# Kernel optimization log

Hardware: AMD Instinct MI355X
Metric: run time of the kernel (lower is better)

Reference implementation:

```python
import jax, jax.numpy as jnp
import numpy as np
import math


def setup_inputs() -> dict:
    key = jax.random.key(0)
    ks = jax.random.split(key, 10)
    b, n, d, h = 2, 1024, 1024, 16
    hd = d // h
    std = 0.02
    x = jax.random.normal(ks[0], (b, n, d), jnp.float32)
    Wq = jax.random.normal(ks[1], (d, d), jnp.float32) * std
    Wk = jax.random.normal(ks[2], (d, d), jnp.float32) * std
    Wv = jax.random.normal(ks[3], (d, d), jnp.float32) * std
    Wo = jax.random.normal(ks[4], (d, d), jnp.float32) * std
    Ww1 = jax.random.normal(ks[5], (d, hd), jnp.float32) * std
    Ww2 = jax.random.normal(ks[6], (hd, d), jnp.float32) * std
    Wb = jax.random.normal(ks[7], (d, h), jnp.float32) * std
    Wf = jax.random.normal(ks[8], (d, h), jnp.float32) * std
    # delta initialized so sigmoid(delta) = threshold = 0.99
    delta = jnp.full((h,), math.log(0.99 / (1.0 - 0.99)), jnp.float32)
    return dict(x=x, Wq=Wq, Wk=Wk, Wv=Wv, Wo=Wo, Ww1=Ww1, Ww2=Ww2, Wb=Wb, Wf=Wf, delta=delta)


def reference(x, Wq, Wk, Wv, Wo, Ww1, Ww2, Wb, Wf, delta):
    b, n, d = x.shape
    h = delta.shape[0]
    hd = d // h
    scale = hd ** -0.5
    q = (x @ Wq).reshape(b, n, h, hd)
    k = (x @ Wk).reshape(b, n, h, hd)
    v = (x @ Wv).reshape(b, n, h, hd)
    w = ((x @ Ww1) @ Ww2).reshape(b, n, h, hd)
    # l2-normalize write directions per head
    w = w * jax.lax.rsqrt(jnp.sum(w * w, axis=-1, keepdims=True) + 1e-6)
    beta = 2.0 * jax.nn.sigmoid(x @ Wb)                      # (b,n,h)
    log_f = jax.nn.log_sigmoid((x @ Wf + delta).astype(jnp.float32))  # (b,n,h)
    bt = jnp.transpose(beta, (0, 2, 1))                      # (b,h,n)
    # PaTH attention: logit_{t,j} = q_t^T H_t H_{t-1} ... H_{j+1} k_j, H_s = I - beta_s w_s w_s^T.
    # UT transform: c_{s,j} = w_s . k_j^{(s-1)} satisfies (I + L) C = tril(W K^T, -1)
    # with L_{s,r} = beta_r (w_s . w_r) for r < s.
    A = jnp.einsum('bshd,brhd->bhsr', w, w)                  # w_s . w_r
    L = jnp.tril(A, -1) * bt[:, :, None, :]                  # (b,h,n,n), strictly lower
    Mlow = jnp.tril(jnp.einsum('bshd,bjhd->bhsj', w, k), -1)
    C = jax.scipy.linalg.solve_triangular(L, Mlow, lower=True, unit_diagonal=True)
    # transformed score: S_{t,j} = q_t.k_j - sum_{j<s<=t} beta_s (q_t.w_s) c_{s,j}
    G = jnp.tril(jnp.einsum('bthd,bshd->bhts', q, w) * bt[:, :, None, :])
    S = jnp.einsum('bthd,bjhd->bhtj', q, k) - G @ C          # (b,h,n,n)
    # forgetting-gate decay: add F_t - F_j (cumulative log-sigmoid gates)
    Fc = jnp.cumsum(jnp.transpose(log_f, (0, 2, 1)), axis=-1)  # (b,h,n)
    logits = S * scale + Fc[..., :, None] - Fc[..., None, :]
    mask = jnp.tril(jnp.ones((n, n), bool))
    logits = jnp.where(mask, logits, -jnp.inf)
    P = jax.nn.softmax(logits, axis=-1)
    o = jnp.einsum('bhtj,bjhd->bthd', P, v).reshape(b, n, d)
    return o @ Wo
```

## Files before the change

kernel.cpp:

```cpp
#include <hip/hip_runtime.h>
#include <hip/hip_bf16.h>

#define DEV static __device__ __forceinline__

constexpr float SM_SCALE = 0.125f;

typedef __attribute__((ext_vector_type(8))) short s16x8;
typedef __attribute__((ext_vector_type(8))) unsigned short u16x8;
typedef __attribute__((ext_vector_type(4))) unsigned short u16x4;
typedef __attribute__((ext_vector_type(4))) float f32x4;

DEV float bf2f(unsigned short u) {
  union { unsigned int i; float f; } v; v.i = ((unsigned int)u) << 16; return v.f;
}
DEV unsigned short f2bf(float f) {
  union { float f; unsigned int i; } v; v.f = f;
  unsigned int r = v.i + 0x7fffu + ((v.i >> 16) & 1u);
  return (unsigned short)(r >> 16);
}
DEV void tri_unrank(int r, int& k, int& i) {
  k = (int)((sqrtf(8.f * r + 1.f) - 1.f) * 0.5f);
  while (k * (k + 1) / 2 > r) --k;
  while ((k + 1) * (k + 2) / 2 <= r) ++k;
  i = r - k * (k + 1) / 2;
}
DEV void glds16(const void* g, void* l) {
  __builtin_amdgcn_global_load_lds(
      (const __attribute__((address_space(1))) void*)g,
      (__attribute__((address_space(3))) void*)l, 16, 0, 0);
}
DEV void pipe_drain_barrier() {
  asm volatile("s_waitcnt vmcnt(0)" ::: "memory");
  __builtin_amdgcn_s_barrier();
}

constexpr size_t OFF_XB   = 0;
constexpr size_t OFF_WQT  = 4194304;
constexpr size_t OFF_WKT  = 6291456;
constexpr size_t OFF_WVT  = 8388608;
constexpr size_t OFF_WOT  = 10485760;
constexpr size_t OFF_W1C  = 12582912;
constexpr size_t OFF_W2T  = 12713984;
constexpr size_t OFF_BETA = 12582912;
constexpr size_t OFF_Q16  = 12845056;
constexpr size_t OFF_K16  = 17039360;
constexpr size_t OFF_VT   = 21233664;
constexpr size_t OFF_WN16 = 25427968;
constexpr size_t OFF_WB16 = 29622272;
constexpr size_t OFF_WNF  = 33816576;
constexpr size_t OFF_OB   = 33816576;
constexpr size_t OFF_BFT  = 38010880;
constexpr size_t OFF_FC   = 38273024;
constexpr size_t OFF_L    = 38404096;
constexpr size_t OFF_CT   = 105512960;
constexpr size_t OFF_G    = 172621824;
constexpr size_t OFF_BL   = 239730688;
constexpr size_t OFF_U128 = 244187136;
constexpr size_t OFF_B256 = 252575744;

__global__ __launch_bounds__(256) void prep_all(
    const float* __restrict__ W0, const float* __restrict__ W1,
    const float* __restrict__ W2, const float* __restrict__ W3,
    const float* __restrict__ Ww1, const float* __restrict__ Ww2,
    const float* __restrict__ x, const float* __restrict__ Wb,
    const float* __restrict__ Wf,
    unsigned short* __restrict__ D0, unsigned short* __restrict__ D1,
    unsigned short* __restrict__ D2, unsigned short* __restrict__ D3,
    unsigned short* __restrict__ W1c, unsigned short* __restrict__ W2T,
    unsigned short* __restrict__ xb, unsigned short* __restrict__ BFT) {
  int bidx = blockIdx.x;
  int t = threadIdx.x;
  if (bidx >= 2096) {
    int e0 = ((bidx - 2096) * 256 + t) * 8;
    int j = e0 >> 10, i0 = e0 & 1023;
    u16x8 o;
#pragma unroll
    for (int e = 0; e < 8; ++e) {
      int i = i0 + e;
      float v = 0.f;
      if (j < 16) v = Wb[i * 16 + j];
      else if (j < 32) v = Wf[i * 16 + (j - 16)];
      o[e] = f2bf(v);
    }
    *(u16x8*)(BFT + e0) = o;
    return;
  }
  if (bidx >= 2064) {
    int i = ((bidx - 2064) * 256 + t) * 8;
    float4 a = *(const float4*)(Ww1 + i);
    float4 b = *(const float4*)(Ww1 + i + 4);
    u16x8 o;
    o[0] = f2bf(a.x); o[1] = f2bf(a.y); o[2] = f2bf(a.z); o[3] = f2bf(a.w);
    o[4] = f2bf(b.x); o[5] = f2bf(b.y); o[6] = f2bf(b.z); o[7] = f2bf(b.w);
    *(u16x8*)(W1c + i) = o;
    return;
  }
  if (bidx >= 1040) {
    int i = ((bidx - 1040) * 256 + t) * 8;
    float4 a = *(const float4*)(x + i);
    float4 b = *(const float4*)(x + i + 4);
    u16x8 o;
    o[0] = f2bf(a.x); o[1] = f2bf(a.y); o[2] = f2bf(a.z); o[3] = f2bf(a.w);
    o[4] = f2bf(b.x); o[5] = f2bf(b.y); o[6] = f2bf(b.z); o[7] = f2bf(b.w);
    *(u16x8*)(xb + i) = o;
    return;
  }
  const float* src; unsigned short* dst; int R, C, c0, r0;
  if (bidx >= 1024) {
    src = Ww2; dst = W2T; R = 64; C = 1024;
    c0 = (bidx - 1024) * 64; r0 = 0;
  } else {
    int z = bidx >> 8, xy = bidx & 255;
    src = z == 0 ? W0 : z == 1 ? W1 : z == 2 ? W2 : W3;
    dst = z == 0 ? D0 : z == 1 ? D1 : z == 2 ? D2 : D3;
    R = 1024; C = 1024;
    c0 = (xy & 15) * 64; r0 = (xy >> 4) * 64;
  }
  __shared__ float tile[64 * 65];
#pragma unroll
  for (int i = 0; i < 16; ++i) {
    int lin = t + i * 256; int r = lin >> 6, c = lin & 63;
    tile[r * 65 + c] = src[(size_t)(r0 + r) * C + c0 + c];
  }
  __syncthreads();
#pragma unroll
  for (int i = 0; i < 16; ++i) {
    int lin = t + i * 256; int c = lin >> 6, r = lin & 63;
    dst[(size_t)(c0 + c) * R + r0 + r] = f2bf(tile[r * 65 + c]);
  }
}

__global__ __launch_bounds__(256) void bgfc(const float* __restrict__ BL,
    const float* __restrict__ delta, float* __restrict__ Beta, float* __restrict__ Fc) {
  int bh = blockIdx.x;
  int b = bh >> 4, h = bh & 15;
  int t = threadIdx.x;
  __shared__ float buf[1024];
  __shared__ float tsum[256];
  float dh = delta[h];
#pragma unroll
  for (int i = 0; i < 4; ++i) {
    int n = t + i * 256;
    int row = (b << 10) + n;
    float braw = BL[row * 64 + h];
    Beta[row * 16 + h] = 2.f / (1.f + __expf(-braw));
    float lraw = BL[row * 64 + 16 + h] + dh;
    buf[n] = (lraw >= 0.f) ? -log1pf(__expf(-lraw)) : (lraw - log1pf(__expf(lraw)));
  }
  __syncthreads();
  float loc[4]; float run = 0.f;
#pragma unroll
  for (int i = 0; i < 4; ++i) { run += buf[t * 4 + i]; loc[i] = run; }
  tsum[t] = run;
  __syncthreads();
  for (int off = 1; off < 256; off <<= 1) {
    float add = (t >= off) ? tsum[t - off] : 0.f;
    __syncthreads();
    tsum[t] += add;
    __syncthreads();
  }
  float excl = tsum[t] - run;
#pragma unroll
  for (int i = 0; i < 4; ++i) Fc[bh * 1024 + t * 4 + i] = excl + loc[i];
}

__global__ __launch_bounds__(256) void proj_big(const unsigned short* __restrict__ xb,
    const unsigned short* __restrict__ WqT, const unsigned short* __restrict__ WkT,
    const unsigned short* __restrict__ WvT, const unsigned short* __restrict__ WfT,
    const unsigned short* __restrict__ BFT,
    unsigned short* __restrict__ Q16, unsigned short* __restrict__ K16,
    unsigned short* __restrict__ VT, unsigned short* __restrict__ WNF,
    float* __restrict__ BL) {
  int sg = blockIdx.x;
  int virt = (sg % 8) * 66 + (sg / 8);
  const unsigned short *A, *BT; unsigned short* out = nullptr; int m0, n0;
  int mode = 0;
  if (virt < 256) {
    int g = virt >> 4, in = virt & 15;
    int ssb = g >> 2, gin = g & 3;
    int mb = (ssb >> 1) * 2 + (gin >> 1);
    int nb = (ssb & 1) * 2 + (gin & 1);
    int my = mb * 4 + (in >> 2);
    int nx = nb * 4 + (in & 3);
    m0 = my * 128; A = xb;
    if (nx < 8) { BT = WqT; out = Q16; n0 = nx * 128; }
    else { BT = WkT; out = K16; n0 = (nx - 8) * 128; }
  } else if (virt < 384) {
    int r = virt - 256; int bz = r >> 6; int rr = r & 63;
    int g = rr >> 4, in = rr & 15;
    int my = (g >> 1) * 4 + (in >> 2);
    int nx = (g & 1) * 4 + (in & 3);
    m0 = my * 128; n0 = nx * 128;
    A = WvT; BT = xb + ((size_t)bz << 20); out = VT + ((size_t)bz << 20);
  } else if (virt < 512) {
    int r = virt - 384;
    int g = r >> 4, in = r & 15;
    int my = (g >> 1) * 4 + (in >> 2);
    int nx = (g & 1) * 4 + (in & 3);
    m0 = my * 128; n0 = nx * 128;
    A = xb; BT = WfT; out = WNF;
  } else {
    m0 = (virt - 512) * 128; n0 = 0;
    A = xb; BT = BFT; mode = 1;
  }
  int t = threadIdx.x;
  int w = t >> 6, l = t & 63;
  int wr = w >> 1, wc = w & 1;
  int fr = l & 15, fq = l >> 4;
  __shared__ unsigned short As[2 * 8192];
  __shared__ unsigned short Bs[2 * 8192];
  f32x4 acc[4][4];
#pragma unroll
  for (int m = 0; m < 4; ++m)
#pragma unroll
    for (int c = 0; c < 4; ++c) acc[m][c] = (f32x4){0.f, 0.f, 0.f, 0.f};

#define STAGE_PB(buf, k0) {                                             \
  _Pragma("unroll")                                                     \
  for (int i = 0; i < 4; ++i) {                                         \
    int cid = t + i * 256;                                              \
    int row = cid >> 3, ch = cid & 7;                                   \
    int chs = ch ^ (row & 7);                                           \
    glds16(A + (size_t)(m0 + row) * 1024 + (k0) + chs * 8, (char*)(As + (buf) * 8192) + cid * 16); \
    glds16(BT + (size_t)(n0 + row) * 1024 + (k0) + chs * 8, (char*)(Bs + (buf) * 8192) + cid * 16); \
  } }

  STAGE_PB(0, 0);
  pipe_drain_barrier();
  int cur = 0;
  for (int kt = 0; kt < 16; ++kt) {
    if (kt < 15) STAGE_PB(cur ^ 1, (kt + 1) * 64);
    const char* Ab = (const char*)(As + cur * 8192);
    const char* Bb = (const char*)(Bs + cur * 8192);
    __builtin_amdgcn_s_setprio(1);
#pragma unroll
    for (int kh = 0; kh < 2; ++kh) {
      s16x8 af[4], bfv[4];
#pragma unroll
      for (int m = 0; m < 4; ++m) {
        int ra = wr * 64 + 16 * m + fr;
        af[m] = *(const s16x8*)(Ab + (((ra << 7) + (kh << 6) + (fq << 4)) ^ ((ra & 7) << 4)));
      }
#pragma unroll
      for (int c = 0; c < 4; ++c) {
        int rb = wc * 64 + 16 * c + fr;
        bfv[c] = *(const s16x8*)(Bb + (((rb << 7) + (kh << 6) + (fq << 4)) ^ ((rb & 7) << 4)));
      }
#pragma unroll
      for (int m = 0; m < 4; ++m)
#pragma unroll
        for (int c = 0; c < 4; ++c)
          acc[m][c] = __builtin_amdgcn_mfma_f32_16x16x32_bf16(af[m], bfv[c], acc[m][c], 0, 0, 0);
    }
    __builtin_amdgcn_s_setprio(0);
    pipe_drain_barrier();
    cur ^= 1;
  }
#undef STAGE_PB
#pragma unroll
  for (int m = 0; m < 4; ++m) {
#pragma unroll
    for (int c = 0; c < 4; ++c) {
      int col = n0 + wc * 64 + 16 * c + fr;
#pragma unroll
      for (int r = 0; r < 4; ++r) {
        int grow = m0 + wr * 64 + 16 * m + fq * 4 + r;
        if (mode == 0) out[(size_t)grow * 1024 + col] = f2bf(acc[m][c][r]);
        else if (col < 64) BL[(size_t)grow * 64 + col] = acc[m][c][r];
      }
    }
  }
}

template<int F32OUT>
__global__ __launch_bounds__(256) void gemm_nt(const unsigned short* __restrict__ A,
    const unsigned short* __restrict__ BT, void* __restrict__ out,
    int M, int N, int K) {
  __shared__ unsigned short As[2 * 4096];
  __shared__ unsigned short Bs[2 * 4096];
  int m0 = blockIdx.y * 64, n0 = blockIdx.x * 64;
  int t = threadIdx.x;
  int w = t >> 6, l = t & 63, fr = l & 15;
  int koB = (l >> 4) * 16;
  f32x4 acc[4];
#pragma unroll
  for (int c = 0; c < 4; ++c) acc[c] = (f32x4){0.f, 0.f, 0.f, 0.f};

#define STAGE_G(buf, k0) {                                              \
  _Pragma("unroll")                                                     \
  for (int i = 0; i < 2; ++i) {                                         \
    int cid = t + i * 256;                                              \
    int row = cid >> 3, ch = cid & 7;                                   \
    int chs = ch ^ (row & 7);                                           \
    glds16(A + (size_t)(m0 + row) * K + (k0) + chs * 8, (char*)(As + (buf) * 4096) + cid * 16); \
    glds16(BT + (size_t)(n0 + row) * K + (k0) + chs * 8, (char*)(Bs + (buf) * 4096) + cid * 16); \
  } }

  int nt = K >> 6;
  STAGE_G(0, 0);
  pipe_drain_barrier();
  int cur = 0;
  for (int kt = 0; kt < nt; ++kt) {
    if (kt + 1 < nt) STAGE_G(cur ^ 1, (kt + 1) * 64);
    const char* Ab = (const char*)(As + cur * 4096);
    const char* Bb = (const char*)(Bs + cur * 4096);
    __builtin_amdgcn_s_setprio(1);
#pragma unroll
    for (int kh = 0; kh < 2; ++kh) {
      int ra = 16 * w + fr;
      s16x8 a = *(const s16x8*)(Ab + (((ra << 7) + (kh << 6) + koB) ^ ((ra & 7) << 4)));
#pragma unroll
      for (int c = 0; c < 4; ++c) {
        int rb = 16 * c + fr;
        s16x8 bb = *(const s16x8*)(Bb + (((rb << 7) + (kh << 6) + koB) ^ ((rb & 7) << 4)));
        acc[c] = __builtin_amdgcn_mfma_f32_16x16x32_bf16(a, bb, acc[c], 0, 0, 0);
      }
    }
    __builtin_amdgcn_s_setprio(0);
    pipe_drain_barrier();
    cur ^= 1;
  }
#undef STAGE_G
  int rbase = m0 + 16 * w + ((l >> 4) << 2);
#pragma unroll
  for (int c = 0; c < 4; ++c) {
    int col = n0 + 16 * c + fr;
#pragma unroll
    for (int r = 0; r < 4; ++r) {
      if (F32OUT) ((float*)out)[(size_t)(rbase + r) * N + col] = acc[c][r];
      else ((unsigned short*)out)[(size_t)(rbase + r) * N + col] = f2bf(acc[c][r]);
    }
  }
}

__global__ __launch_bounds__(256) void gemm_outproj(const unsigned short* __restrict__ A,
    const unsigned short* __restrict__ BT, float* __restrict__ out) {
  int sg = blockIdx.x;
  int virt = (sg & 7) * 64 + (sg >> 3);
  int g = virt >> 6, in = virt & 63;
  int my = (g >> 1) * 8 + (in >> 3);
  int nx = (g & 1) * 8 + (in & 7);
  int m0 = my * 64, n0 = nx * 64;
  const int K = 1024, N = 1024;
  __shared__ unsigned short As[2 * 4096];
  __shared__ unsigned short Bs[2 * 4096];
  int t = threadIdx.x;
  int w = t >> 6, l = t & 63, fr = l & 15;
  int koB = (l >> 4) * 16;
  f32x4 acc[4];
#pragma unroll
  for (int c = 0; c < 4; ++c) acc[c] = (f32x4){0.f, 0.f, 0.f, 0.f};

#define STAGE_O(buf, k0) {                                              \
  _Pragma("unroll")                                                     \
  for (int i = 0; i < 2; ++i) {                                         \
    int cid = t + i * 256;                                              \
    int row = cid >> 3, ch = cid & 7;                                   \
    int chs = ch ^ (row & 7);                                           \
    glds16(A + (size_t)(m0 + row) * K + (k0) + chs * 8, (char*)(As + (buf) * 4096) + cid * 16); \
    glds16(BT + (size_t)(n0 + row) * K + (k0) + chs * 8, (char*)(Bs + (buf) * 4096) + cid * 16); \
  } }

  STAGE_O(0, 0);
  pipe_drain_barrier();
  int cur = 0;
  for (int kt = 0; kt < 16; ++kt) {
    if (kt + 1 < 16) STAGE_O(cur ^ 1, (kt + 1) * 64);
    const char* Ab = (const char*)(As + cur * 4096);
    const char* Bb = (const char*)(Bs + cur * 4096);
    __builtin_amdgcn_s_setprio(1);
#pragma unroll
    for (int kh = 0; kh < 2; ++kh) {
      int ra = 16 * w + fr;
      s16x8 a = *(const s16x8*)(Ab + (((ra << 7) + (kh << 6) + koB) ^ ((ra & 7) << 4)));
#pragma unroll
      for (int c = 0; c < 4; ++c) {
        int rb = 16 * c + fr;
        s16x8 bb = *(const s16x8*)(Bb + (((rb << 7) + (kh << 6) + koB) ^ ((rb & 7) << 4)));
        acc[c] = __builtin_amdgcn_mfma_f32_16x16x32_bf16(a, bb, acc[c], 0, 0, 0);
      }
    }
    __builtin_amdgcn_s_setprio(0);
    pipe_drain_barrier();
    cur ^= 1;
  }
#undef STAGE_O
  int rbase = m0 + 16 * w + ((l >> 4) << 2);
#pragma unroll
  for (int c = 0; c < 4; ++c) {
    int col = n0 + 16 * c + fr;
#pragma unroll
    for (int r = 0; r < 4; ++r)
      out[(size_t)(rbase + r) * N + col] = acc[c][r];
  }
}

__global__ __launch_bounds__(256) void wnorm2(const unsigned short* __restrict__ WNF,
    const float* __restrict__ Beta, unsigned short* __restrict__ WN,
    unsigned short* __restrict__ WB) {
  int row = blockIdx.x;
  int wave = threadIdx.x >> 6, lane = threadIdx.x & 63;
#pragma unroll
  for (int i = 0; i < 4; ++i) {
    int hh = wave * 4 + i;
    size_t idx = ((size_t)row << 10) + hh * 64 + lane;
    float v = bf2f(WNF[idx]);
    float ss = v * v;
#pragma unroll
    for (int off = 1; off < 64; off <<= 1) ss += __shfl_xor(ss, off);
    float wn = v * rsqrtf(ss + 1e-6f);
    WN[idx] = f2bf(wn);
    WB[idx] = f2bf(wn * Beta[row * 16 + hh]);
  }
}

__global__ __launch_bounds__(256) void pairLG(const unsigned short* __restrict__ WN,
    const unsigned short* __restrict__ Q, const unsigned short* __restrict__ WB,
    unsigned short* __restrict__ Lg, unsigned short* __restrict__ Gg) {
  int idx = blockIdx.x;
  int bh = idx & 31, r0r = idx >> 5;
  int tb2, jb2; tri_unrank(r0r, tb2, jb2);
  int b = bh >> 4, h = bh & 15;
  int m0 = tb2 * 128, n0 = jb2 * 128;
  int t = threadIdx.x;
  int w = t >> 6, l = t & 63;
  int wr = w >> 1, wc = w & 1;
  int fr = l & 15, fq = l >> 4;
  __shared__ unsigned short As[128 * 64];
  __shared__ unsigned short Bs[128 * 64];
  const unsigned short* WNb = WN + ((size_t)b << 20) + h * 64;
  const unsigned short* Qb  = Q + ((size_t)b << 20) + h * 64;
  const unsigned short* WBb = WB + ((size_t)b << 20) + h * 64;
  size_t base = (size_t)bh << 20;
#pragma unroll
  for (int i = 0; i < 4; ++i) {
    int cid = t + i * 256;
    int row = cid >> 3, ch = cid & 7;
    int chs = ch ^ (row & 7);
    glds16(WNb + ((size_t)(m0 + row) << 10) + chs * 8, (char*)As + cid * 16);
    glds16(WBb + ((size_t)(n0 + row) << 10) + chs * 8, (char*)Bs + cid * 16);
  }
  __syncthreads();
  for (int pass = 0; pass < 2; ++pass) {
    f32x4 acc[4][4];
#pragma unroll
    for (int m = 0; m < 4; ++m)
#pragma unroll
      for (int c = 0; c < 4; ++c) acc[m][c] = (f32x4){0.f, 0.f, 0.f, 0.f};
#pragma unroll
    for (int kh = 0; kh < 2; ++kh) {
      s16x8 af[4], bfv[4];
#pragma unroll
      for (int m = 0; m < 4; ++m) {
        int ra = wr * 64 + 16 * m + fr;
        af[m] = *(const s16x8*)((char*)As + (((ra << 7) + (kh << 6) + (fq << 4)) ^ ((ra & 7) << 4)));
      }
#pragma unroll
      for (int c = 0; c < 4; ++c) {
        int rb = wc * 64 + 16 * c + fr;
        bfv[c] = *(const s16x8*)((char*)Bs + (((rb << 7) + (kh << 6) + (fq << 4)) ^ ((rb & 7) << 4)));
      }
#pragma unroll
      for (int m = 0; m < 4; ++m)
#pragma unroll
        for (int c = 0; c < 4; ++c)
          acc[m][c] = __builtin_amdgcn_mfma_f32_16x16x32_bf16(af[m], bfv[c], acc[m][c], 0, 0, 0);
    }
    unsigned short* dst = pass ? Gg : Lg;
#pragma unroll
    for (int m = 0; m < 4; ++m) {
#pragma unroll
      for (int c = 0; c < 4; ++c) {
        int gj = n0 + wc * 64 + 16 * c + fr;
#pragma unroll
        for (int r = 0; r < 4; ++r) {
          int gi = m0 + wr * 64 + 16 * m + fq * 4 + r;
          bool keep = pass ? (gj <= gi) : (gj < gi);
          dst[base + ((size_t)gi << 10) + gj] = f2bf(keep ? -acc[m][c][r] : 0.f);
        }
      }
    }
    if (pass == 0) {
      __syncthreads();
#pragma unroll
      for (int i = 0; i < 4; ++i) {
        int cid = t + i * 256;
        int row = cid >> 3, ch = cid & 7;
        int chs = ch ^ (row & 7);
        glds16(Qb + ((size_t)(m0 + row) << 10) + chs * 8, (char*)As + cid * 16);
      }
      __syncthreads();
    }
  }
}

__global__ __launch_bounds__(256) void score128s(const unsigned short* __restrict__ Q,
    const unsigned short* __restrict__ Kk, const unsigned short* __restrict__ G,
    const unsigned short* __restrict__ CT, unsigned short* __restrict__ Sg) {
  int idx = blockIdx.x;
  int bh = idx & 31, r0r = idx >> 5;
  int k, i; tri_unrank(r0r, k, i);
  int tb2 = (7 - k) + i, jb2 = i;
  int b = bh >> 4, h = bh & 15;
  int m0 = tb2 * 128, n0 = jb2 * 128;
  int t = threadIdx.x;
  int w = t >> 6, l = t & 63;
  int wr = w >> 1, wc = w & 1;
  int fr = l & 15, fq = l >> 4;
  __shared__ unsigned short As[2 * 8192];
  __shared__ unsigned short Bs[2 * 8192];
  size_t base = (size_t)bh << 20;
  const unsigned short* Qb_ = Q + ((size_t)b << 20) + h * 64;
  const unsigned short* Kb_ = Kk + ((size_t)b << 20) + h * 64;
  const unsigned short* Gb_ = G + base;
  const unsigned short* Cb_ = CT + base;
  int kbase = jb2 * 128;
  int nsteps = 1 + (tb2 - jb2 + 1) * 2;
  f32x4 acc[4][4];
#pragma unroll
  for (int m = 0; m < 4; ++m)
#pragma unroll
    for (int c = 0; c < 4; ++c) acc[m][c] = (f32x4){0.f, 0.f, 0.f, 0.f};

#define STAGE_SC(buf, stp) {                                            \
  const unsigned short* pa; const unsigned short* pb; int koff;         \
  if ((stp) == 0) { pa = Qb_; pb = Kb_; koff = 0; }                     \
  else { pa = Gb_; pb = Cb_; koff = kbase + ((stp) - 1) * 64; }         \
  _Pragma("unroll")                                                     \
  for (int i2 = 0; i2 < 4; ++i2) {                                      \
    int cid = t + i2 * 256;                                             \
    int row = cid >> 3, ch = cid & 7;                                   \
    int chs = ch ^ (row & 7);                                           \
    glds16(pa + ((size_t)(m0 + row) << 10) + koff + chs * 8, (char*)(As + (buf) * 8192) + cid * 16); \
    glds16(pb + ((size_t)(n0 + row) << 10) + koff + chs * 8, (char*)(Bs + (buf) * 8192) + cid * 16); \
  } }

  STAGE_SC(0, 0);
  pipe_drain_barrier();
  int cur = 0;
  for (int step = 0; step < nsteps; ++step) {
    if (step + 1 < nsteps) STAGE_SC(cur ^ 1, step + 1);
    const char* Ab = (const char*)(As + cur * 8192);
    const char* Bb = (const char*)(Bs + cur * 8192);
    __builtin_amdgcn_s_setprio(1);
#pragma unroll
    for (int kh = 0; kh < 2; ++kh) {
      s16x8 af[4], bfv[4];
#pragma unroll
      for (int m = 0; m < 4; ++m) {
        int ra = wr * 64 + 16 * m + fr;
        af[m] = *(const s16x8*)(Ab + (((ra << 7) + (kh << 6) + (fq << 4)) ^ ((ra & 7) << 4)));
      }
#pragma unroll
      for (int c = 0; c < 4; ++c) {
        int rb = wc * 64 + 16 * c + fr;
        bfv[c] = *(const s16x8*)(Bb + (((rb << 7) + (kh << 6) + (fq << 4)) ^ ((rb & 7) << 4)));
      }
#pragma unroll
      for (int m = 0; m < 4; ++m)
#pragma unroll
        for (int c = 0; c < 4; ++c)
          acc[m][c] = __builtin_amdgcn_mfma_f32_16x16x32_bf16(af[m], bfv[c], acc[m][c], 0, 0, 0);
    }
    __builtin_amdgcn_s_setprio(0);
    pipe_drain_barrier();
    cur ^= 1;
  }
#undef STAGE_SC
#pragma unroll
  for (int m = 0; m < 4; ++m) {
#pragma unroll
    for (int c = 0; c < 4; ++c) {
      int gj = n0 + wc * 64 + 16 * c + fr;
#pragma unroll
      for (int r = 0; r < 4; ++r) {
        int gi = m0 + wr * 64 + 16 * m + fq * 4 + r;
        Sg[base + ((size_t)gi << 10) + gj] = f2bf(acc[m][c][r]);
      }
    }
  }
}

__global__ __launch_bounds__(256) void invbuild(const unsigned short* __restrict__ Lb,
    unsigned short* __restrict__ U128) {
  int ib = blockIdx.x, bh = blockIdx.y;
  int t = threadIdx.x, w = t >> 6, l = t & 63, fr = l & 15, fq = l >> 4;
  int s0 = ib * 128;
  size_t base = (size_t)bh << 20;
  unsigned short* Uo = U128 + (((size_t)(bh * 8 + ib)) << 14);
  __shared__ float LD[2][64 * 65];
  __shared__ unsigned short UaR[64 * 72];
  __shared__ unsigned short UcR[64 * 72];
  __shared__ unsigned short UaT[64 * 64];
  __shared__ unsigned short T1T[64 * 64];
#pragma unroll
  for (int i = 0; i < 32; ++i) {
    int lin = t + i * 256;
    int blk = lin >> 12, s = (lin >> 6) & 63, r = lin & 63;
    LD[blk][s * 65 + r] = -bf2f(Lb[base + ((size_t)(s0 + blk * 64 + s) << 10) + s0 + blk * 64 + r]);
  }
  __syncthreads();
  if (t < 128) {
    int blk = t >> 6, j = t & 63;
    const float* ld = LD[blk];
    float cc[64];
#pragma unroll
    for (int s = 0; s < 64; ++s) cc[s] = (s == j) ? 1.f : 0.f;
#pragma unroll
    for (int r = 0; r < 63; ++r) {
      float val = cc[r];
#pragma unroll
      for (int s = r + 1; s < 64; ++s) cc[s] -= ld[s * 65 + r] * val;
    }
    if (blk == 0) {
#pragma unroll
      for (int s = 0; s < 64; ++s) {
        unsigned short v = f2bf(cc[s]);
        UaR[s * 72 + j] = v;
        *(unsigned short*)((char*)UaT + (((j << 7) + (s << 1)) ^ ((j & 7) << 4))) = v;
      }
    } else {
#pragma unroll
      for (int s = 0; s < 64; ++s) UcR[s * 72 + j] = f2bf(cc[s]);
    }
  }
  __syncthreads();
#pragma unroll
  for (int i = 0; i < 8; ++i) {
    int cid = t + i * 256;
    int row = cid >> 4, ch = cid & 15;
    u16x8 v = {0, 0, 0, 0, 0, 0, 0, 0};
    if (row < 64) {
      if (ch < 8) {
#pragma unroll
        for (int e = 0; e < 8; ++e) v[e] = UaR[row * 72 + ch * 8 + e];
      }
      *(u16x8*)(Uo + row * 128 + ch * 8) = v;
    } else if (ch >= 8) {
#pragma unroll
      for (int e = 0; e < 8; ++e) v[e] = UcR[(row - 64) * 72 + (ch - 8) * 8 + e];
      *(u16x8*)(Uo + row * 128 + ch * 8) = v;
    }
  }
  f32x4 a1[4];
#pragma unroll
  for (int c = 0; c < 4; ++c) a1[c] = (f32x4){0.f, 0.f, 0.f, 0.f};
#pragma unroll
  for (int kc = 0; kc < 2; ++kc) {
    s16x8 af = *(const s16x8*)(Lb + base + ((size_t)(s0 + 64 + 16 * w + fr) << 10) + s0 + kc * 32 + fq * 8);
#pragma unroll
    for (int c = 0; c < 4; ++c) {
      int j = 16 * c + fr;
      s16x8 bb = *(const s16x8*)((char*)UaT + (((j << 7) + (kc << 6) + (fq << 4)) ^ ((j & 7) << 4)));
      a1[c] = __builtin_amdgcn_mfma_f32_16x16x32_bf16(af, bb, a1[c], 0, 0, 0);
    }
  }
#pragma unroll
  for (int c = 0; c < 4; ++c) {
    int gj = 16 * c + fr;
    int sb = 16 * w + fq * 4;
    u16x4 pk;
#pragma unroll
    for (int r = 0; r < 4; ++r) pk[r] = f2bf(a1[c][r]);
    *(u16x4*)((char*)T1T + (((gj << 7) + (sb << 1)) ^ ((gj & 7) << 4))) = pk;
  }
  __syncthreads();
  f32x4 a2[4];
#pragma unroll
  for (int c = 0; c < 4; ++c) a2[c] = (f32x4){0.f, 0.f, 0.f, 0.f};
#pragma unroll
  for (int kc = 0; kc < 2; ++kc) {
    s16x8 af = *(const s16x8*)(UcR + (16 * w + fr) * 72 + kc * 32 + fq * 8);
#pragma unroll
    for (int c = 0; c < 4; ++c) {
      int j = 16 * c + fr;
      s16x8 bb = *(const s16x8*)((char*)T1T + (((j << 7) + (kc << 6) + (fq << 4)) ^ ((j & 7) << 4)));
      a2[c] = __builtin_amdgcn_mfma_f32_16x16x32_bf16(af, bb, a2[c], 0, 0, 0);
    }
  }
#pragma unroll
  for (int c = 0; c < 4; ++c) {
    int gj = 16 * c + fr;
#pragma unroll
    for (int r = 0; r < 4; ++r)
      Uo[(64 + 16 * w + fq * 4 + r) * 128 + gj] = f2bf(a2[c][r]);
  }
}

__global__ __launch_bounds__(256) void u256build(const unsigned short* __restrict__ Lb,
    const unsigned short* __restrict__ U128, unsigned short* __restrict__ B256) {
  int qb = blockIdx.x, bh = blockIdx.y;
  int t = threadIdx.x, w = t >> 6, l = t & 63, fr = l & 15, fq = l >> 4;
  int s0 = qb * 256;
  size_t base = (size_t)bh << 20;
  const unsigned short* Ua = U128 + (((size_t)(bh * 8 + 2 * qb)) << 14);
  const unsigned short* Uc = U128 + (((size_t)(bh * 8 + 2 * qb + 1)) << 14);
  unsigned short* out = B256 + (((size_t)(bh * 4 + qb)) << 14);
  __shared__ unsigned short UaT[16384];
  __shared__ unsigned short T1T[16384];
#pragma unroll
  for (int i = 0; i < 8; ++i) {
    int cid = t + i * 256;
    int s = cid >> 4, ch = cid & 15;
    u16x8 v = *(const u16x8*)(Ua + s * 128 + ch * 8);
#pragma unroll
    for (int e = 0; e < 8; ++e) {
      int j = ch * 8 + e;
      int byt = ((j << 8) + (s << 1)) ^ ((j & 15) << 4);
      *(unsigned short*)((char*)UaT + byt) = v[e];
    }
  }
  __syncthreads();
  f32x4 a1[2][8];
#pragma unroll
  for (int m = 0; m < 2; ++m)
#pragma unroll
    for (int c = 0; c < 8; ++c) a1[m][c] = (f32x4){0.f, 0.f, 0.f, 0.f};
#pragma unroll
  for (int kc = 0; kc < 4; ++kc) {
    s16x8 af[2];
#pragma unroll
    for (int m = 0; m < 2; ++m)
      af[m] = *(const s16x8*)(Lb + base + ((size_t)(s0 + 128 + 32 * w + 16 * m + fr) << 10) + s0 + kc * 32 + fq * 8);
#pragma unroll
    for (int c = 0; c < 8; ++c) {
      int j = 16 * c + fr;
      s16x8 bb = *(const s16x8*)((char*)UaT + (((j << 8) + (kc << 6) + (fq << 4)) ^ ((j & 15) << 4)));
#pragma unroll
      for (int m = 0; m < 2; ++m)
        a1[m][c] = __builtin_amdgcn_mfma_f32_16x16x32_bf16(af[m], bb, a1[m][c], 0, 0, 0);
    }
  }
#pragma unroll
  for (int m = 0; m < 2; ++m) {
#pragma unroll
    for (int c = 0; c < 8; ++c) {
      int col = 16 * c + fr;
      int row0 = 32 * w + 16 * m + fq * 4;
      u16x4 pk;
#pragma unroll
      for (int r = 0; r < 4; ++r) pk[r] = f2bf(a1[m][c][r]);
      int byt = ((col << 8) + (row0 << 1)) ^ ((col & 15) << 4);
      *(u16x4*)((char*)T1T + byt) = pk;
    }
  }
  __syncthreads();
  f32x4 a2[2][8];
#pragma unroll
  for (int m = 0; m < 2; ++m)
#pragma unroll
    for (int c = 0; c < 8; ++c) a2[m][c] = (f32x4){0.f, 0.f, 0.f, 0.f};
#pragma unroll
  for (int kc = 0; kc < 4; ++kc) {
    s16x8 af[2];
#pragma unroll
    for (int m = 0; m < 2; ++m)
      af[m] = *(const s16x8*)(Uc + (32 * w + 16 * m + fr) * 128 + kc * 32 + fq * 8);
#pragma unroll
    for (int c = 0; c < 8; ++c) {
      int j = 16 * c + fr;
      s16x8 bb = *(const s16x8*)((char*)T1T + (((j << 8) + (kc << 6) + (fq << 4)) ^ ((j & 15) << 4)));
#pragma unroll
      for (int m = 0; m < 2; ++m)
        a2[m][c] = __builtin_amdgcn_mfma_f32_16x16x32_bf16(af[m], bb, a2[m][c], 0, 0, 0);
    }
  }
#pragma unroll
  for (int m = 0; m < 2; ++m) {
#pragma unroll
    for (int c = 0; c < 8; ++c) {
      int col = 16 * c + fr;
#pragma unroll
      for (int r = 0; r < 4; ++r)
        out[(32 * w + 16 * m + fq * 4 + r) * 128 + col] = f2bf(a2[m][c][r]);
    }
  }
}

__global__ __launch_bounds__(256) void solve256(const unsigned short* __restrict__ WN,
    const unsigned short* __restrict__ Kk, const unsigned short* __restrict__ Lb,
    const unsigned short* __restrict__ U128, const unsigned short* __restrict__ B256,
    unsigned short* __restrict__ CT, int ib) {
  int jb = blockIdx.x, bh = blockIdx.y;
  int b = bh >> 4, h = bh & 15;
  int t = threadIdx.x, w = t >> 6, l = t & 63, fr = l & 15, fq = l >> 4;
  int s0 = ib * 256, j0 = jb * 128;
  size_t base = (size_t)bh << 20;
  __shared__ unsigned short sh[49152];
  unsigned short* rT = sh;
  const unsigned short* Wb_ = WN + ((size_t)b << 20) + h * 64;
  const unsigned short* Kb_ = Kk + ((size_t)b << 20) + h * 64;

  f32x4 acc[4][8];
#pragma unroll
  for (int m = 0; m < 4; ++m)
#pragma unroll
    for (int c = 0; c < 8; ++c) acc[m][c] = (f32x4){0.f, 0.f, 0.f, 0.f};
  int nst = 1 + 4 * ib - 2 * jb; if (nst < 1) nst = 1;

#define STAGE_SV(buf, stp) {                                            \
  int rb = 2 * jb + (stp) - 1;                                          \
  _Pragma("unroll")                                                     \
  for (int i = 0; i < 8; ++i) {                                         \
    int cid = t + i * 256;                                              \
    int row = cid >> 3, ch = cid & 7;                                   \
    int chs = ch ^ (row & 7);                                           \
    const unsigned short* ga = ((stp) == 0)                             \
      ? Wb_ + ((size_t)(s0 + row) << 10) + chs * 8                      \
      : Lb + base + ((size_t)(s0 + row) << 10) + rb * 64 + chs * 8;     \
    glds16(ga, (char*)(sh + (buf) * 16384) + cid * 16);                 \
  }                                                                     \
  _Pragma("unroll")                                                     \
  for (int i = 0; i < 4; ++i) {                                         \
    int cid = t + i * 256;                                              \
    int row = cid >> 3, ch = cid & 7;                                   \
    int chs = ch ^ (row & 7);                                           \
    const unsigned short* gb = ((stp) == 0)                             \
      ? Kb_ + ((size_t)(j0 + row) << 10) + chs * 8                      \
      : CT + base + ((size_t)(j0 + row) << 10) + rb * 64 + chs * 8;     \
    glds16(gb, (char*)(sh + 32768 + (buf) * 8192) + cid * 16);          \
  } }

  STAGE_SV(0, 0);
  pipe_drain_barrier();
  int cur = 0;
  for (int st = 0; st < nst; ++st) {
    if (st + 1 < nst) STAGE_SV(cur ^ 1, st + 1);
    const char* Ab = (const char*)(sh + cur * 16384);
    const char* Bb = (const char*)(sh + 32768 + cur * 8192);
    __builtin_amdgcn_s_setprio(1);
#pragma unroll
    for (int kh = 0; kh < 2; ++kh) {
      s16x8 af[4], bfv[8];
#pragma unroll
      for (int m = 0; m < 4; ++m) {
        int ra = 64 * w + 16 * m + fr;
        af[m] = *(const s16x8*)(Ab + (((ra << 7) + (kh << 6) + (fq << 4)) ^ ((ra & 7) << 4)));
      }
#pragma unroll
      for (int c = 0; c < 8; ++c) {
        int rb2 = 16 * c + fr;
        bfv[c] = *(const s16x8*)(Bb + (((rb2 << 7) + (kh << 6) + (fq << 4)) ^ ((rb2 & 7) << 4)));
      }
#pragma unroll
      for (int m = 0; m < 4; ++m)
#pragma unroll
        for (int c = 0; c < 8; ++c)
          acc[m][c] = __builtin_amdgcn_mfma_f32_16x16x32_bf16(af[m], bfv[c], acc[m][c], 0, 0, 0);
    }
    __builtin_amdgcn_s_setprio(0);
    pipe_drain_barrier();
    cur ^= 1;
  }
#undef STAGE_SV
#pragma unroll
  for (int m = 0; m < 4; ++m) {
#pragma unroll
    for (int c = 0; c < 8; ++c) {
      int sl0 = 64 * w + 16 * m + fq * 4;
      int jl = 16 * c + fr;
      u16x4 pk;
#pragma unroll
      for (int r = 0; r < 4; ++r) {
        float v = acc[m][c][r];
        if (j0 + jl >= s0 + sl0 + r) v = 0.f;
        pk[r] = f2bf(v);
      }
      int byt = ((jl << 9) + (sl0 << 1)) ^ ((jl & 15) << 4);
      *(u16x4*)((char*)rT + byt) = pk;
    }
  }
  __syncthreads();
  const unsigned short* Ua = U128 + (((size_t)(bh * 8 + 2 * ib)) << 14);
  const unsigned short* Uc = U128 + (((size_t)(bh * 8 + 2 * ib + 1)) << 14);
  const unsigned short* Bm = B256 + (((size_t)(bh * 4 + ib)) << 14);
#pragma unroll
  for (int m = 0; m < 4; ++m)
#pragma unroll
    for (int c = 0; c < 8; ++c) acc[m][c] = (f32x4){0.f, 0.f, 0.f, 0.f};
  int nkc = (w < 2) ? 4 : 8;
  for (int kc = 0; kc < nkc; ++kc) {
    const unsigned short* src; int arow;
    if (w < 2) { src = Ua; arow = 64 * w; }
    else { src = (kc < 4) ? Bm : Uc; arow = 64 * (w - 2); }
    s16x8 uf[4];
#pragma unroll
    for (int m = 0; m < 4; ++m)
      uf[m] = *(const s16x8*)(src + (arow + 16 * m + fr) * 128 + (kc & 3) * 32 + fq * 8);
#pragma unroll
    for (int c = 0; c < 8; ++c) {
      int jl = 16 * c + fr;
      s16x8 bb = *(const s16x8*)((char*)rT + (((jl << 9) + (kc << 6) + (fq << 4)) ^ ((jl & 15) << 4)));
#pragma unroll
      for (int m = 0; m < 4; ++m)
        acc[m][c] = __builtin_amdgcn_mfma_f32_16x16x32_bf16(uf[m], bb, acc[m][c], 0, 0, 0);
    }
  }
#pragma unroll
  for (int m = 0; m < 4; ++m) {
#pragma unroll
    for (int c = 0; c < 8; ++c) {
      int jl = 16 * c + fr;
      int sb = 64 * w + 16 * m + fq * 4;
      u16x4 pk;
#pragma unroll
      for (int r = 0; r < 4; ++r) pk[r] = f2bf(acc[m][c][r]);
      *(u16x4*)(CT + base + ((size_t)(j0 + jl) << 10) + s0 + sb) = pk;
    }
  }
}

__global__ __launch_bounds__(256) void pv_kernel(const unsigned short* __restrict__ S,
    const unsigned short* __restrict__ VT, const float* __restrict__ Fc,
    unsigned short* __restrict__ Ob) {
  int idx = blockIdx.x;
  int bh = idx & 31, rank = idx >> 5;
  int tb = 15 - rank;
  int b = bh >> 4, h = bh & 15;
  int t0 = tb * 64;
  int t = threadIdx.x, w = t >> 6, l = t & 63, fr = l & 15, fq = l >> 4;
  int g = l >> 3, ch = l & 7;
  __shared__ unsigned short Pl[4][16 * 64];
  size_t base = (size_t)bh << 20;
  float m0 = -1e30f, m1 = -1e30f, l0 = 0.f, l1 = 0.f;
  f32x4 acc[4];
#pragma unroll
  for (int c = 0; c < 4; ++c) acc[c] = (f32x4){0.f,0.f,0.f,0.f};
  for (int jb = 0; jb <= tb; ++jb) {
    int j0 = jb * 64;
    float sc[2];
#pragma unroll
    for (int i = 0; i < 2; ++i) {
      int row16 = g + i * 8;
      int row64 = 16 * w + row16;
      int grow = t0 + row64;
      u16x8 sv = *(const u16x8*)(S + base + ((size_t)grow << 10) + j0 + ch * 8);
      float4 f0 = *(const float4*)(Fc + bh * 1024 + j0 + ch * 8);
      float4 f1 = *(const float4*)(Fc + bh * 1024 + j0 + ch * 8 + 4);
      float vals[8];
      float tm = -1e30f;
#pragma unroll
      for (int e = 0; e < 8; ++e) {
        float fc = e < 4 ? ((const float*)&f0)[e] : ((const float*)&f1)[e - 4];
        float v = bf2f(sv[e]) * SM_SCALE - fc;
        if (jb == tb && ch * 8 + e > row64) v = -1e30f;
        vals[e] = v; tm = fmaxf(tm, v);
      }
      tm = fmaxf(tm, __shfl_xor(tm, 1));
      tm = fmaxf(tm, __shfl_xor(tm, 2));
      tm = fmaxf(tm, __shfl_xor(tm, 4));
      float mo = i ? m1 : m0;
      float mn = fmaxf(mo, tm);
      float s = __expf(mo - mn);
      u16x8 pv;
      float psum = 0.f;
#pragma unroll
      for (int e = 0; e < 8; ++e) {
        float p = __expf(vals[e] - mn);
        psum += p; pv[e] = f2bf(p);
      }
      int byt = ((row16 << 7) + (ch << 4)) ^ ((row16 & 7) << 4);
      *(u16x8*)((char*)Pl[w] + byt) = pv;
      psum += __shfl_xor(psum, 1);
      psum += __shfl_xor(psum, 2);
      psum += __shfl_xor(psum, 4);
      if (i) { m1 = mn; l1 = l1 * s + psum; } else { m0 = mn; l0 = l0 * s + psum; }
      sc[i] = s;
    }
    __builtin_amdgcn_wave_barrier();
    float cr[4];
#pragma unroll
    for (int r = 0; r < 4; ++r) {
      int rho = fq * 4 + r;
      int src = (rho & 7) * 8;
      float v0 = __shfl(sc[0], src);
      float v1 = __shfl(sc[1], src);
      cr[r] = (rho < 8) ? v0 : v1;
    }
#pragma unroll
    for (int c = 0; c < 4; ++c)
#pragma unroll
      for (int r = 0; r < 4; ++r) acc[c][r] *= cr[r];
#pragma unroll
    for (int kh = 0; kh < 2; ++kh) {
      s16x8 a = *(const s16x8*)((char*)Pl[w] + (((fr << 7) + (kh << 6) + (fq << 4)) ^ ((fr & 7) << 4)));
#pragma unroll
      for (int c = 0; c < 4; ++c) {
        s16x8 bb = *(const s16x8*)(VT + ((size_t)bh * 64 + 16 * c + fr) * 1024 + j0 + kh * 32 + fq * 8);
        acc[c] = __builtin_amdgcn_mfma_f32_16x16x32_bf16(a, bb, acc[c], 0, 0, 0);
      }
    }
    __builtin_amdgcn_wave_barrier();
  }
  float inv[4];
#pragma unroll
  for (int r = 0; r < 4; ++r) {
    int rho = fq * 4 + r;
    int src = (rho & 7) * 8;
    float v0 = __shfl(l0, src);
    float v1 = __shfl(l1, src);
    inv[r] = 1.f / ((rho < 8) ? v0 : v1);
  }
#pragma unroll
  for (int c = 0; c < 4; ++c) {
#pragma unroll
    for (int r = 0; r < 4; ++r) {
      int grow = t0 + 16 * w + fq * 4 + r;
      Ob[((size_t)(b * 1024) + grow) * 1024 + h * 64 + 16 * c + fr] = f2bf(acc[c][r] * inv[r]);
    }
  }
}

extern "C" void kernel_launch(void* const* d_in, const int* in_sizes, int n_in,
                              void* d_out, int out_size, void* d_ws, size_t ws_size,
                              hipStream_t stream) {
  const float* x    = (const float*)d_in[0];
  const float* Wq   = (const float*)d_in[1];
  const float* Wk   = (const float*)d_in[2];
  const float* Wv   = (const float*)d_in[3];
  const float* Wo   = (const float*)d_in[4];
  const float* Ww1  = (const float*)d_in[5];
  const float* Ww2  = (const float*)d_in[6];
  const float* Wb   = (const float*)d_in[7];
  const float* Wf   = (const float*)d_in[8];
  const float* delta= (const float*)d_in[9];

  char* ws = (char*)d_ws;
  unsigned short* xb   = (unsigned short*)(ws + OFF_XB);
  unsigned short* WqT  = (unsigned short*)(ws + OFF_WQT);
  unsigned short* WkT  = (unsigned short*)(ws + OFF_WKT);
  unsigned short* WvT  = (unsigned short*)(ws + OFF_WVT);
  unsigned short* WoT  = (unsigned short*)(ws + OFF_WOT);
  unsigned short* W1c  = (unsigned short*)(ws + OFF_W1C);
  unsigned short* W2T  = (unsigned short*)(ws + OFF_W2T);
  float*          Beta = (float*)(ws + OFF_BETA);
  unsigned short* Q16  = (unsigned short*)(ws + OFF_Q16);
  unsigned short* K16  = (unsigned short*)(ws + OFF_K16);
  unsigned short* VT   = (unsigned short*)(ws + OFF_VT);
  unsigned short* WN16 = (unsigned short*)(ws + OFF_WN16);
  unsigned short* WB16 = (unsigned short*)(ws + OFF_WB16);
  unsigned short* WNF16= (unsigned short*)(ws + OFF_WNF);
  unsigned short* ObB  = (unsigned short*)(ws + OFF_OB);
  unsigned short* BFT  = (unsigned short*)(ws + OFF_BFT);
  float*          Fc   = (float*)(ws + OFF_FC);
  unsigned short* Lbuf = (unsigned short*)(ws + OFF_L);
  unsigned short* Sbuf = (unsigned short*)(ws + OFF_L);
  unsigned short* CT   = (unsigned short*)(ws + OFF_CT);
  unsigned short* Gbuf = (unsigned short*)(ws + OFF_G);
  float*          BL   = (float*)(ws + OFF_BL);
  unsigned short* U128 = (unsigned short*)(ws + OFF_U128);
  unsigned short* B256 = (unsigned short*)(ws + OFF_B256);

  dim3 blk(256);
  prep_all<<<2160, blk, 0, stream>>>(Wq, Wk, Wv, Wo, Ww1, Ww2, x, Wb, Wf,
                                     WqT, WkT, WvT, WoT, W1c, W2T, xb, BFT);
  gemm_nt<0><<<dim3(16,16), blk, 0, stream>>>(W2T, W1c, WN16, 1024, 1024, 64);
  proj_big<<<528, blk, 0, stream>>>(xb, WqT, WkT, WvT, WN16, BFT,
                                    Q16, K16, VT, WNF16, BL);
  bgfc<<<32, blk, 0, stream>>>(BL, delta, Beta, Fc);
  wnorm2<<<2048, blk, 0, stream>>>(WNF16, Beta, WN16, WB16);
  pairLG<<<dim3(36 * 32), blk, 0, stream>>>(WN16, Q16, WB16, Lbuf, Gbuf);
  invbuild<<<dim3(8,32), blk, 0, stream>>>(Lbuf, U128);
  u256build<<<dim3(4,32), blk, 0, stream>>>(Lbuf, U128, B256);
  for (int ib = 0; ib < 4; ++ib)
    solve256<<<dim3(2 * ib + 2, 32), blk, 0, stream>>>(WN16, K16, Lbuf, U128, B256, CT, ib);
  score128s<<<dim3(36 * 32), blk, 0, stream>>>(Q16, K16, Gbuf, CT, Sbuf);
  pv_kernel<<<dim3(512), blk, 0, stream>>>(Sbuf, VT, Fc, ObB);
  gemm_outproj<<<512, blk, 0, stream>>>(ObB, WoT, (float*)d_out);
}
```

Baseline: 289.0 us.

## Enlarge proj_big tiles to 256x128 and halve the grid

```diff
diff --git a/kernel.cpp b/kernel.cpp
--- a/kernel.cpp
+++ b/kernel.cpp
@@ -172,57 +172,52 @@
     unsigned short* __restrict__ VT, unsigned short* __restrict__ WNF,
     float* __restrict__ BL) {
   int sg = blockIdx.x;
-  int virt = (sg % 8) * 66 + (sg / 8);
+  int virt = (sg % 8) * 33 + (sg / 8);
   const unsigned short *A, *BT; unsigned short* out = nullptr; int m0, n0;
   int mode = 0;
-  if (virt < 256) {
-    int g = virt >> 4, in = virt & 15;
-    int ssb = g >> 2, gin = g & 3;
-    int mb = (ssb >> 1) * 2 + (gin >> 1);
-    int nb = (ssb & 1) * 2 + (gin & 1);
-    int my = mb * 4 + (in >> 2);
-    int nx = nb * 4 + (in & 3);
-    m0 = my * 128; A = xb;
+  if (virt < 128) {
+    int my = virt >> 4, nx = virt & 15;
+    m0 = my * 256; A = xb;
     if (nx < 8) { BT = WqT; out = Q16; n0 = nx * 128; }
     else { BT = WkT; out = K16; n0 = (nx - 8) * 128; }
-  } else if (virt < 384) {
-    int r = virt - 256; int bz = r >> 6; int rr = r & 63;
-    int g = rr >> 4, in = rr & 15;
-    int my = (g >> 1) * 4 + (in >> 2);
-    int nx = (g & 1) * 4 + (in & 3);
-    m0 = my * 128; n0 = nx * 128;
+  } else if (virt < 192) {
+    int r = virt - 128; int bz = r >> 5; int rr = r & 31;
+    m0 = (rr >> 3) * 256; n0 = (rr & 7) * 128;
     A = WvT; BT = xb + ((size_t)bz << 20); out = VT + ((size_t)bz << 20);
-  } else if (virt < 512) {
-    int r = virt - 384;
-    int g = r >> 4, in = r & 15;
-    int my = (g >> 1) * 4 + (in >> 2);
-    int nx = (g & 1) * 4 + (in & 3);
-    m0 = my * 128; n0 = nx * 128;
+  } else if (virt < 256) {
+    int r = virt - 192;
+    m0 = (r >> 3) * 256; n0 = (r & 7) * 128;
     A = xb; BT = WfT; out = WNF;
   } else {
-    m0 = (virt - 512) * 128; n0 = 0;
+    m0 = (virt - 256) * 256; n0 = 0;
     A = xb; BT = BFT; mode = 1;
   }
   int t = threadIdx.x;
   int w = t >> 6, l = t & 63;
-  int wr = w >> 1, wc = w & 1;
   int fr = l & 15, fq = l >> 4;
-  __shared__ unsigned short As[2 * 8192];
-  __shared__ unsigned short Bs[2 * 8192];
-  f32x4 acc[4][4];
+  __shared__ unsigned short sh[49152];
+  f32x4 acc[4][8];
 #pragma unroll
   for (int m = 0; m < 4; ++m)
 #pragma unroll
-    for (int c = 0; c < 4; ++c) acc[m][c] = (f32x4){0.f, 0.f, 0.f, 0.f};
+    for (int c = 0; c < 8; ++c) acc[m][c] = (f32x4){0.f, 0.f, 0.f, 0.f};
 
 #define STAGE_PB(buf, k0) {                                             \
+  _Pragma("unroll")                                                     \
+  for (int i = 0; i < 8; ++i) {                                         \
+    int cid = t + i * 256;                                              \
+    int row = cid >> 3, ch = cid & 7;                                   \
+    int chs = ch ^ (row & 7);                                           \
+    glds16(A + (size_t)(m0 + row) * 1024 + (k0) + chs * 8,              \
+           (char*)(sh + (buf) * 16384) + cid * 16);                     \
+  }                                                                     \
   _Pragma("unroll")                                                     \
   for (int i = 0; i < 4; ++i) {                                         \
     int cid = t + i * 256;                                              \
     int row = cid >> 3, ch = cid & 7;                                   \
     int chs = ch ^ (row & 7);                                           \
-    glds16(A + (size_t)(m0 + row) * 1024 + (k0) + chs * 8, (char*)(As + (buf) * 8192) + cid * 16); \
-    glds16(BT + (size_t)(n0 + row) * 1024 + (k0) + chs * 8, (char*)(Bs + (buf) * 8192) + cid * 16); \
+    glds16(BT + (size_t)(n0 + row) * 1024 + (k0) + chs * 8,             \
+           (char*)(sh + 32768 + (buf) * 8192) + cid * 16);              \
   } }
 
   STAGE_PB(0, 0);
@@ -230,27 +225,25 @@
   int cur = 0;
   for (int kt = 0; kt < 16; ++kt) {
     if (kt < 15) STAGE_PB(cur ^ 1, (kt + 1) * 64);
-    const char* Ab = (const char*)(As + cur * 8192);
-    const char* Bb = (const char*)(Bs + cur * 8192);
+    const char* Ab = (const char*)(sh + cur * 16384);
+    const char* Bb = (const char*)(sh + 32768 + cur * 8192);
     __builtin_amdgcn_s_setprio(1);
 #pragma unroll
     for (int kh = 0; kh < 2; ++kh) {
-      s16x8 af[4], bfv[4];
+      s16x8 af[4];
 #pragma unroll
       for (int m = 0; m < 4; ++m) {
-        int ra = wr * 64 + 16 * m + fr;
+        int ra = 64 * w + 16 * m + fr;
         af[m] = *(const s16x8*)(Ab + (((ra << 7) + (kh << 6) + (fq << 4)) ^ ((ra & 7) << 4)));
       }
 #pragma unroll
-      for (int c = 0; c < 4; ++c) {
-        int rb = wc * 64 + 16 * c + fr;
-        bfv[c] = *(const s16x8*)(Bb + (((rb << 7) + (kh << 6) + (fq << 4)) ^ ((rb & 7) << 4)));
-      }
-#pragma unroll
-      for (int m = 0; m < 4; ++m)
-#pragma unroll
-        for (int c = 0; c < 4; ++c)
-          acc[m][c] = __builtin_amdgcn_mfma_f32_16x16x32_bf16(af[m], bfv[c], acc[m][c], 0, 0, 0);
+      for (int c = 0; c < 8; ++c) {
+        int rb = 16 * c + fr;
+        s16x8 bb = *(const s16x8*)(Bb + (((rb << 7) + (kh << 6) + (fq << 4)) ^ ((rb & 7) << 4)));
+#pragma unroll
+        for (int m = 0; m < 4; ++m)
+          acc[m][c] = __builtin_amdgcn_mfma_f32_16x16x32_bf16(af[m], bb, acc[m][c], 0, 0, 0);
+      }
     }
     __builtin_amdgcn_s_setprio(0);
     pipe_drain_barrier();
@@ -260,11 +253,11 @@
 #pragma unroll
   for (int m = 0; m < 4; ++m) {
 #pragma unroll
-    for (int c = 0; c < 4; ++c) {
-      int col = n0 + wc * 64 + 16 * c + fr;
+    for (int c = 0; c < 8; ++c) {
+      int col = n0 + 16 * c + fr;
 #pragma unroll
       for (int r = 0; r < 4; ++r) {
-        int grow = m0 + wr * 64 + 16 * m + fq * 4 + r;
+        int grow = m0 + 64 * w + 16 * m + fq * 4 + r;
         if (mode == 0) out[(size_t)grow * 1024 + col] = f2bf(acc[m][c][r]);
         else if (col < 64) BL[(size_t)grow * 64 + col] = acc[m][c][r];
       }
@@ -1055,7 +1048,7 @@
   prep_all<<<2160, blk, 0, stream>>>(Wq, Wk, Wv, Wo, Ww1, Ww2, x, Wb, Wf,
                                      WqT, WkT, WvT, WoT, W1c, W2T, xb, BFT);
   gemm_nt<0><<<dim3(16,16), blk, 0, stream>>>(W2T, W1c, WN16, 1024, 1024, 64);
-  proj_big<<<528, blk, 0, stream>>>(xb, WqT, WkT, WvT, WN16, BFT,
+  proj_big<<<264, blk, 0, stream>>>(xb, WqT, WkT, WvT, WN16, BFT,
                                     Q16, K16, VT, WNF16, BL);
   bgfc<<<32, blk, 0, stream>>>(BL, delta, Beta, Fc);
   wnorm2<<<2048, blk, 0, stream>>>(WNF16, Beta, WN16, WB16);
```

New measurement: 307.3 us. 1.06x slower.
